# Kernel optimization log

Measured on AMD Instinct MI355X. Metric: run time of the kernel, lower is better.

Reference implementation:

```python
import jax, jax.numpy as jnp
import numpy as np

B, T, IN, H, OUT = 4096, 7, 512, 1024, 512


def setup_inputs() -> dict:
    key = jax.random.key(0)
    ks = jax.random.split(key, 13)
    s = 0.05  # weight init scale to keep gates/tanh unsaturated
    return {
        "x": jax.random.normal(ks[0], (B, T, IN), jnp.float32),
        "W_ih1": jax.random.normal(ks[1], (3 * H, IN), jnp.float32) * s,
        "W_hh1": jax.random.normal(ks[2], (3 * H, H), jnp.float32) * s,
        "b_ih1": jax.random.normal(ks[3], (3 * H,), jnp.float32) * s,
        "b_hh1": jax.random.normal(ks[4], (3 * H,), jnp.float32) * s,
        "W_ih2": jax.random.normal(ks[5], (3 * H, H), jnp.float32) * s,
        "W_hh2": jax.random.normal(ks[6], (3 * H, H), jnp.float32) * s,
        "b_ih2": jax.random.normal(ks[7], (3 * H,), jnp.float32) * s,
        "b_hh2": jax.random.normal(ks[8], (3 * H,), jnp.float32) * s,
        "Wo1": jax.random.normal(ks[9], (OUT, H), jnp.float32) * s,
        "bo1": jax.random.normal(ks[10], (OUT,), jnp.float32) * s,
        "Wo2": jax.random.normal(ks[11], (OUT, H), jnp.float32) * s,
        "bo2": jax.random.normal(ks[12], (OUT,), jnp.float32) * s,
    }


def gru_cell(x, h, W_ih, W_hh, b_ih, b_hh):
    # torch.nn.GRUCell math, gate order (r, z, n)
    gi = x @ W_ih.T + b_ih          # [B, 3H]
    gh = h @ W_hh.T + b_hh          # [B, 3H]
    i_r, i_z, i_n = jnp.split(gi, 3, axis=-1)
    h_r, h_z, h_n = jnp.split(gh, 3, axis=-1)
    r = jax.nn.sigmoid(i_r + h_r)
    z = jax.nn.sigmoid(i_z + h_z)
    n = jnp.tanh(i_n + r * h_n)
    return (1.0 - z) * n + z * h


def reference(x, W_ih1, W_hh1, b_ih1, b_hh1, W_ih2, W_hh2, b_ih2, b_hh2,
              Wo1, bo1, Wo2, bo2):
    batch = x.shape[0]
    h1_0 = jnp.zeros((batch, H), x.dtype)
    h2_0 = jnp.zeros((batch, H), x.dtype)

    def step(carry, x_t):
        h1, h2 = carry
        h1 = gru_cell(x_t, h1, W_ih1, W_hh1, b_ih1, b_hh1)
        h2 = gru_cell(h1, h2, W_ih2, W_hh2, b_ih2, b_hh2)
        out = jnp.tanh(h1 @ Wo1.T + bo1) + jnp.tanh(h2 @ Wo2.T + bo2)
        # s_t_cached starts as T zeros and only T steps run, so the popped
        # cached state is always zeros: mse(h2, 0) == mean(h2**2)
        aux = jnp.mean(jnp.square(h2))
        return (h1, h2), (out, aux)

    xs = jnp.swapaxes(x, 0, 1)  # [T, B, IN]
    _, (outs, auxs) = jax.lax.scan(step, (h1_0, h2_0), xs)
    outputs = jnp.swapaxes(outs, 0, 1)  # [B, T, OUT]
    aux_loss = jnp.sum(auxs)
    return outputs, aux_loss
```

## Files before the change

kernel.cpp:

```cpp
#include <hip/hip_runtime.h>
#include <cstdint>

#define BB   4096
#define TT   7
#define INF  512
#define HH   1024
#define OUTF 512
#define G3   3072

typedef short bf16x8 __attribute__((ext_vector_type(8)));
typedef float f32x4  __attribute__((ext_vector_type(4)));

static __device__ __forceinline__ unsigned short f2bf(float f) {
  unsigned u = __float_as_uint(f);
  unsigned r = ((u >> 16) & 1u) + 0x7FFFu;
  return (unsigned short)((u + r) >> 16);
}
static __device__ __forceinline__ float bf2f(unsigned short s) {
  return __uint_as_float(((unsigned)s) << 16);
}

#define GLDS16(gp, lp)                                                        \
  __builtin_amdgcn_global_load_lds(                                           \
      (const __attribute__((address_space(1))) void*)(gp),                    \
      (__attribute__((address_space(3))) void*)(lp), 16, 0, 0)

__device__ __forceinline__ int xcd_swz(int bid, int nwg) {
  return (bid & 7) * (nwg >> 3) + (bid >> 3);
}

__global__ __launch_bounds__(256)
void cvt_f32_to_bf16_x4(const float* __restrict__ in, unsigned short* __restrict__ out, int n4) {
  int i = blockIdx.x * 256 + threadIdx.x;
  if (i >= n4) return;
  const float4 v = ((const float4*)in)[i];
  ushort4 o;
  o.x = f2bf(v.x); o.y = f2bf(v.y); o.z = f2bf(v.z); o.w = f2bf(v.w);
  ((ushort4*)out)[i] = o;
}

template<int BM, int BN, int WM, int WN, int GN>
__device__ __forceinline__ void gemm_core(
    const unsigned short* __restrict__ A, long lda, long bm,
    const unsigned short* __restrict__ Wp, long ldw, int K,
    const float* __restrict__ biasp,
    void* __restrict__ Cp, long ldc,
    const float* __restrict__ addp, long ldadd, int mode)
{
  constexpr int ABUF = BM * 32;
  constexpr int WBUF = BN * 32;
  constexpr int AR = (BM * 4) / 256;
  constexpr int WR = (BN * 4) / 256;
  __shared__ __attribute__((aligned(16))) unsigned short sm[2 * (ABUF + WBUF)];
  unsigned short* As = sm;
  unsigned short* Ws = sm + 2 * ABUF;
  __attribute__((address_space(3))) unsigned short* lAs =
      (__attribute__((address_space(3))) unsigned short*)As;
  __attribute__((address_space(3))) unsigned short* lWs =
      (__attribute__((address_space(3))) unsigned short*)Ws;

  const int tid  = threadIdx.x;
  const int lane = tid & 63;
  const int wid  = tid >> 6;
  const int wr = (wid / GN) * (WM * 16);
  const int wc = (wid % GN) * (WN * 16);
  const int fr = lane & 15;
  const int fk = (lane >> 4) * 8;

  const unsigned short* gpa[AR];
  const unsigned short* gpw[WR];
  int lofa[AR], lofw[WR];
#pragma unroll
  for (int r = 0; r < AR; ++r) {
    const int c = r * 256 + tid;
    gpa[r] = A + (bm + (c >> 2)) * lda + (c & 3) * 8;
    lofa[r] = c * 8;
  }
#pragma unroll
  for (int r = 0; r < WR; ++r) {
    const int c = r * 256 + tid;
    gpw[r] = Wp + (long)(c >> 2) * ldw + (c & 3) * 8;
    lofw[r] = c * 8;
  }

#define STAGE(buf, kt) do {                                                   \
    _Pragma("unroll")                                                         \
    for (int r = 0; r < AR; ++r) GLDS16(gpa[r] + (kt), lAs + (buf) * ABUF + lofa[r]); \
    _Pragma("unroll")                                                         \
    for (int r = 0; r < WR; ++r) GLDS16(gpw[r] + (kt), lWs + (buf) * WBUF + lofw[r]); \
  } while (0)

  f32x4 acc[WM][WN] = {};
  STAGE(0, 0);
  __syncthreads();
  const int NK = K >> 5;
  for (int it = 0; it < NK; ++it) {
    const int cur = it & 1;
    if (it + 1 < NK) STAGE(cur ^ 1, (it + 1) << 5);
    bf16x8 af[WM], wf[WN];
#pragma unroll
    for (int i = 0; i < WM; ++i)
      af[i] = *(const bf16x8*)&As[cur * ABUF + (wr + i * 16 + fr) * 32 + fk];
#pragma unroll
    for (int i = 0; i < WN; ++i)
      wf[i] = *(const bf16x8*)&Ws[cur * WBUF + (wc + i * 16 + fr) * 32 + fk];
#pragma unroll
    for (int mi = 0; mi < WM; ++mi)
#pragma unroll
      for (int ni = 0; ni < WN; ++ni)
        acc[mi][ni] = __builtin_amdgcn_mfma_f32_16x16x32_bf16(af[mi], wf[ni], acc[mi][ni], 0, 0, 0);
    __syncthreads();
  }
#undef STAGE

  const int q = lane >> 4;
#pragma unroll
  for (int ni = 0; ni < WN; ++ni) {
    const int col = wc + ni * 16 + fr;
    const float bv = biasp[col];
#pragma unroll
    for (int mi = 0; mi < WM; ++mi) {
      const long row = bm + wr + mi * 16 + q * 4;
#pragma unroll
      for (int j = 0; j < 4; ++j) {
        const float v = acc[mi][ni][j] + bv;
        if (mode == 0)      ((float*)Cp)[(row + j) * ldc + col] = v;
        else if (mode == 1) ((float*)Cp)[(row + j) * ldc + col] = tanhf(v);
        else if (mode == 2) ((float*)Cp)[(row + j) * ldc + col] = tanhf(v) + addp[(row + j) * ldadd + col];
        else                ((unsigned short*)Cp)[(row + j) * ldc + col] = f2bf(v);
      }
    }
  }
}

__global__ __launch_bounds__(256)
void k_gi1(const unsigned short* __restrict__ A, long lda,
           const unsigned short* __restrict__ W, const float* __restrict__ bias,
           unsigned short* __restrict__ C, int gx)
{
  const int wg = xcd_swz(blockIdx.x, gridDim.x);
  const int bx = wg % gx, by = wg / gx;
  gemm_core<128,128,4,4,2>(A, lda, (long)bx * 128, W + (long)by * 128 * INF, INF, INF,
                           bias + by * 128, C + by * 128, G3, nullptr, 0, 3);
}

__global__ __launch_bounds__(256)
void k_gh_dual(const unsigned short* __restrict__ h1b, const unsigned short* __restrict__ h2b,
               const unsigned short* __restrict__ W1, const unsigned short* __restrict__ W2,
               const float* __restrict__ b1, const float* __restrict__ b2,
               float* __restrict__ gh1, float* __restrict__ gh2)
{
  const int wg = xcd_swz(blockIdx.x, gridDim.x);
  const int bx = wg % 32;
  const int by = (wg / 32) % 24;
  const int z  = wg / (32 * 24);
  const unsigned short* Aa = z ? h2b : h1b;
  const unsigned short* Ww = (z ? W2 : W1) + (long)by * 128 * HH;
  const float* bias = (z ? b2 : b1) + by * 128;
  float* C = (z ? gh2 : gh1) + by * 128;
  gemm_core<128,128,4,4,2>(Aa, HH, (long)bx * 128, Ww, HH, HH, bias, C, G3, nullptr, 0, 0);
}

__global__ __launch_bounds__(256)
void k_gi2_o1(const unsigned short* __restrict__ h1b,
              const unsigned short* __restrict__ Wih2, const float* __restrict__ bih2,
              float* __restrict__ gi2,
              const unsigned short* __restrict__ Wo1, const float* __restrict__ bo1,
              float* __restrict__ o1t)
{
  const int wg = xcd_swz(blockIdx.x, gridDim.x);
  const int bx = wg % 32;
  const int by = wg / 32;
  const bool g = (by < 24);
  const int bo = by - 24;
  const unsigned short* Ww = g ? (Wih2 + (long)by * 128 * HH) : (Wo1 + (long)bo * 128 * HH);
  const float* bias        = g ? (bih2 + by * 128)            : (bo1 + bo * 128);
  void* C                  = g ? (void*)(gi2 + by * 128)      : (void*)(o1t + bo * 128);
  const long ldc           = g ? (long)G3 : (long)OUTF;
  gemm_core<128,128,4,4,2>(h1b, HH, (long)bx * 128, Ww, HH, HH, bias, C, ldc,
                           nullptr, 0, g ? 0 : 1);
}

__global__ __launch_bounds__(256)
void k_o2_out(const unsigned short* __restrict__ h2b,
              const unsigned short* __restrict__ Wo2, const float* __restrict__ bo2,
              const float* __restrict__ o1t, float* __restrict__ outp)
{
  const int wg = xcd_swz(blockIdx.x, gridDim.x);
  const int bx = wg % 64;
  const int by = wg / 64;
  gemm_core<64,64,2,2,2>(h2b, HH, (long)bx * 64, Wo2 + (long)by * 64 * HH, HH, HH,
                         bo2 + by * 64, outp + by * 64, (long)TT * OUTF,
                         o1t + by * 64, OUTF, 2);
}

template<bool GIBF>
__global__ __launch_bounds__(256)
void k_gate(const void* __restrict__ gi, long gistride,
            const float* __restrict__ gh,
            unsigned short* __restrict__ hb,
            float* __restrict__ auxp)
{
  const int i4 = blockIdx.x * 256 + threadIdx.x;
  const int e  = i4 << 2;
  const int b = e >> 10;
  const int c = e & 1023;
  f32x4 ir, iz, inn;
  if (GIBF) {
    const unsigned short* g = (const unsigned short*)gi + (long)b * gistride + c;
    const ushort4 a0 = *(const ushort4*)(g);
    const ushort4 a1 = *(const ushort4*)(g + HH);
    const ushort4 a2 = *(const ushort4*)(g + 2 * HH);
    ir  = f32x4{bf2f(a0.x), bf2f(a0.y), bf2f(a0.z), bf2f(a0.w)};
    iz  = f32x4{bf2f(a1.x), bf2f(a1.y), bf2f(a1.z), bf2f(a1.w)};
    inn = f32x4{bf2f(a2.x), bf2f(a2.y), bf2f(a2.z), bf2f(a2.w)};
  } else {
    const float* g = (const float*)gi + (long)b * gistride + c;
    ir = *(const f32x4*)g; iz = *(const f32x4*)(g + HH); inn = *(const f32x4*)(g + 2 * HH);
  }
  const float* ghp = gh + (long)b * G3 + c;
  const f32x4 hr = *(const f32x4*)ghp;
  const f32x4 hz = *(const f32x4*)(ghp + HH);
  const f32x4 hn = *(const f32x4*)(ghp + 2 * HH);
  const ushort4 ho = *(const ushort4*)(hb + e);
  const f32x4 h = f32x4{bf2f(ho.x), bf2f(ho.y), bf2f(ho.z), bf2f(ho.w)};
  f32x4 hnew;
  float vsum = 0.f;
#pragma unroll
  for (int j = 0; j < 4; ++j) {
    const float r = 1.f / (1.f + __expf(-(ir[j] + hr[j])));
    const float z = 1.f / (1.f + __expf(-(iz[j] + hz[j])));
    const float n = tanhf(inn[j] + r * hn[j]);
    hnew[j] = (1.f - z) * n + z * h[j];
    vsum += hnew[j] * hnew[j];
  }
  ushort4 o;
  o.x = f2bf(hnew[0]); o.y = f2bf(hnew[1]); o.z = f2bf(hnew[2]); o.w = f2bf(hnew[3]);
  *(ushort4*)(hb + e) = o;
  if (auxp != nullptr) {
#pragma unroll
    for (int off = 32; off > 0; off >>= 1) vsum += __shfl_down(vsum, off);
    __shared__ float wsum[4];
    if ((threadIdx.x & 63) == 0) wsum[threadIdx.x >> 6] = vsum;
    __syncthreads();
    if (threadIdx.x == 0) auxp[blockIdx.x] = wsum[0] + wsum[1] + wsum[2] + wsum[3];
  }
}

__global__ __launch_bounds__(256)
void aux_reduce(const float* __restrict__ p, int n, float* __restrict__ out, float scale) {
  float s = 0.f;
  for (int i = threadIdx.x; i < n; i += 256) s += p[i];
#pragma unroll
  for (int off = 32; off > 0; off >>= 1) s += __shfl_down(s, off);
  __shared__ float wsum[4];
  if ((threadIdx.x & 63) == 0) wsum[threadIdx.x >> 6] = s;
  __syncthreads();
  if (threadIdx.x == 0) out[0] = (wsum[0] + wsum[1] + wsum[2] + wsum[3]) * scale;
}

extern "C" void kernel_launch(void* const* d_in, const int* in_sizes, int n_in,
                              void* d_out, int out_size, void* d_ws, size_t ws_size,
                              hipStream_t stream) {
  const float* x    = (const float*)d_in[0];
  const float* Wih1 = (const float*)d_in[1];
  const float* Whh1 = (const float*)d_in[2];
  const float* bih1 = (const float*)d_in[3];
  const float* bhh1 = (const float*)d_in[4];
  const float* Wih2 = (const float*)d_in[5];
  const float* Whh2 = (const float*)d_in[6];
  const float* bih2 = (const float*)d_in[7];
  const float* bhh2 = (const float*)d_in[8];
  const float* Wo1  = (const float*)d_in[9];
  const float* bo1  = (const float*)d_in[10];
  const float* Wo2  = (const float*)d_in[11];
  const float* bo2  = (const float*)d_in[12];

  char* ws = (char*)d_ws;
  size_t off = 0;
  auto alloc = [&](size_t bytes) {
    char* p = ws + off;
    off = (off + bytes + 255) & ~(size_t)255;
    return p;
  };

  unsigned short* xb    = (unsigned short*)alloc((size_t)BB * TT * INF * 2);
  unsigned short* wih1b = (unsigned short*)alloc((size_t)G3 * INF * 2);
  unsigned short* whh1b = (unsigned short*)alloc((size_t)G3 * HH * 2);
  unsigned short* wih2b = (unsigned short*)alloc((size_t)G3 * HH * 2);
  unsigned short* whh2b = (unsigned short*)alloc((size_t)G3 * HH * 2);
  unsigned short* wo1b  = (unsigned short*)alloc((size_t)OUTF * HH * 2);
  unsigned short* wo2b  = (unsigned short*)alloc((size_t)OUTF * HH * 2);
  unsigned short* h1b = (unsigned short*)alloc((size_t)BB * HH * 2);
  unsigned short* h2b = (unsigned short*)alloc((size_t)BB * HH * 2);
  float* gh1  = (float*)alloc((size_t)BB * G3 * 4);
  float* gh2  = (float*)alloc((size_t)BB * G3 * 4);
  float* o1t  = (float*)alloc((size_t)BB * OUTF * 4);
  float* auxp = (float*)alloc((size_t)TT * (BB * HH / 1024) * 4);
  float* gi2  = gh1;

  const size_t gi1_big   = (size_t)BB * TT * G3 * 2;
  const size_t gi1_small = (size_t)BB * G3 * 2;
  const bool hoist = (off + gi1_big + (size_t)(32 << 20)) <= ws_size;
  unsigned short* gi1b = (unsigned short*)alloc(hoist ? gi1_big : gi1_small);

  float* aux = (float*)d_out + (size_t)BB * TT * OUTF;

  auto cvt = [&](const float* src, unsigned short* dst, size_t n) {
    int n4 = (int)(n / 4);
    cvt_f32_to_bf16_x4<<<dim3((n4 + 255) / 256), dim3(256), 0, stream>>>(src, dst, n4);
  };
  cvt(x,    xb,    (size_t)BB * TT * INF);
  cvt(Wih1, wih1b, (size_t)G3 * INF);
  cvt(Whh1, whh1b, (size_t)G3 * HH);
  cvt(Wih2, wih2b, (size_t)G3 * HH);
  cvt(Whh2, whh2b, (size_t)G3 * HH);
  cvt(Wo1,  wo1b,  (size_t)OUTF * HH);
  cvt(Wo2,  wo2b,  (size_t)OUTF * HH);

  hipMemsetAsync(h1b, 0, (size_t)BB * HH * 2, stream);
  hipMemsetAsync(h2b, 0, (size_t)BB * HH * 2, stream);

  const dim3 blk(256);
  const int gateGrid = BB * HH / 1024;

  if (hoist)
    k_gi1<<<dim3(224 * 24), blk, 0, stream>>>(xb, INF, wih1b, bih1, gi1b, 224);

  for (int t = 0; t < TT; ++t) {
    if (!hoist)
      k_gi1<<<dim3(32 * 24), blk, 0, stream>>>(xb + (size_t)t * INF, (long)TT * INF,
                                               wih1b, bih1, gi1b, 32);
    k_gh_dual<<<dim3(32 * 24 * 2), blk, 0, stream>>>(h1b, h2b, whh1b, whh2b, bhh1, bhh2, gh1, gh2);
    k_gate<true><<<dim3(gateGrid), blk, 0, stream>>>(
        hoist ? gi1b + (size_t)t * G3 : gi1b, hoist ? (long)TT * G3 : (long)G3,
        gh1, h1b, nullptr);
    k_gi2_o1<<<dim3(32 * 28), blk, 0, stream>>>(h1b, wih2b, bih2, gi2, wo1b, bo1, o1t);
    k_gate<false><<<dim3(gateGrid), blk, 0, stream>>>(gi2, (long)G3, gh2, h2b,
                                                      auxp + (size_t)t * gateGrid);
    k_o2_out<<<dim3(64 * 8), blk, 0, stream>>>(h2b, wo2b, bo2, o1t,
                                               (float*)d_out + (size_t)t * OUTF);
  }
  aux_reduce<<<dim3(1), blk, 0, stream>>>(auxp, TT * gateGrid, aux,
                                          1.f / ((float)BB * (float)HH));
}
```

Baseline: 1.568 ms.

## Use single-buffered BK=64 tiles with XOR-swizzled LDS layout in GEMM core

Changes the GEMM mainloop from a double-buffered K=32 pipeline to a single LDS buffer holding K=64 tiles, with two MFMA sub-steps per tile. The global-to-LDS load addresses are XOR-swizzled by row so that the 16-byte fragment reads from LDS avoid bank conflicts on the wider 128-byte rows. This halves the number of barrier iterations and removes bank conflicts, but it gives up overlap of the next tile's load with the current MFMA work, since there is a sync before each load.

```diff
diff --git a/kernel.cpp b/kernel.cpp
--- a/kernel.cpp
+++ b/kernel.cpp
@@ -47,13 +47,11 @@
     void* __restrict__ Cp, long ldc,
     const float* __restrict__ addp, long ldadd, int mode)
 {
-  constexpr int ABUF = BM * 32;
-  constexpr int WBUF = BN * 32;
-  constexpr int AR = (BM * 4) / 256;
-  constexpr int WR = (BN * 4) / 256;
-  __shared__ __attribute__((aligned(16))) unsigned short sm[2 * (ABUF + WBUF)];
+  constexpr int AR = (BM * 8) / 256;
+  constexpr int WR = (BN * 8) / 256;
+  __shared__ __attribute__((aligned(16))) unsigned short sm[(BM + BN) * 64];
   unsigned short* As = sm;
-  unsigned short* Ws = sm + 2 * ABUF;
+  unsigned short* Ws = sm + BM * 64;
   __attribute__((address_space(3))) unsigned short* lAs =
       (__attribute__((address_space(3))) unsigned short*)As;
   __attribute__((address_space(3))) unsigned short* lWs =
@@ -65,53 +63,57 @@
   const int wr = (wid / GN) * (WM * 16);
   const int wc = (wid % GN) * (WN * 16);
   const int fr = lane & 15;
-  const int fk = (lane >> 4) * 8;
+  const int q2 = lane >> 4;
 
   const unsigned short* gpa[AR];
   const unsigned short* gpw[WR];
   int lofa[AR], lofw[WR];
 #pragma unroll
   for (int r = 0; r < AR; ++r) {
-    const int c = r * 256 + tid;
-    gpa[r] = A + (bm + (c >> 2)) * lda + (c & 3) * 8;
-    lofa[r] = c * 8;
+    const int id = r * 256 + tid;
+    const int row = id >> 3, cc = id & 7;
+    gpa[r] = A + (bm + row) * lda + (cc ^ (row & 7)) * 8;
+    lofa[r] = id * 8;
   }
 #pragma unroll
   for (int r = 0; r < WR; ++r) {
-    const int c = r * 256 + tid;
-    gpw[r] = Wp + (long)(c >> 2) * ldw + (c & 3) * 8;
-    lofw[r] = c * 8;
-  }
-
-#define STAGE(buf, kt) do {                                                   \
-    _Pragma("unroll")                                                         \
-    for (int r = 0; r < AR; ++r) GLDS16(gpa[r] + (kt), lAs + (buf) * ABUF + lofa[r]); \
-    _Pragma("unroll")                                                         \
-    for (int r = 0; r < WR; ++r) GLDS16(gpw[r] + (kt), lWs + (buf) * WBUF + lofw[r]); \
-  } while (0)
+    const int id = r * 256 + tid;
+    const int row = id >> 3, cc = id & 7;
+    gpw[r] = Wp + (long)row * ldw + (cc ^ (row & 7)) * 8;
+    lofw[r] = id * 8;
+  }
 
   f32x4 acc[WM][WN] = {};
-  STAGE(0, 0);
-  __syncthreads();
-  const int NK = K >> 5;
-  for (int it = 0; it < NK; ++it) {
-    const int cur = it & 1;
-    if (it + 1 < NK) STAGE(cur ^ 1, (it + 1) << 5);
-    bf16x8 af[WM], wf[WN];
-#pragma unroll
-    for (int i = 0; i < WM; ++i)
-      af[i] = *(const bf16x8*)&As[cur * ABUF + (wr + i * 16 + fr) * 32 + fk];
-#pragma unroll
-    for (int i = 0; i < WN; ++i)
-      wf[i] = *(const bf16x8*)&Ws[cur * WBUF + (wc + i * 16 + fr) * 32 + fk];
-#pragma unroll
-    for (int mi = 0; mi < WM; ++mi)
-#pragma unroll
-      for (int ni = 0; ni < WN; ++ni)
-        acc[mi][ni] = __builtin_amdgcn_mfma_f32_16x16x32_bf16(af[mi], wf[ni], acc[mi][ni], 0, 0, 0);
+  for (int kt = 0; kt < K; kt += 64) {
+    if (kt) __syncthreads();
+#pragma unroll
+    for (int r = 0; r < AR; ++r) GLDS16(gpa[r] + kt, lAs + lofa[r]);
+#pragma unroll
+    for (int r = 0; r < WR; ++r) GLDS16(gpw[r] + kt, lWs + lofw[r]);
     __syncthreads();
-  }
-#undef STAGE
+
+#pragma unroll
+    for (int ks = 0; ks < 2; ++ks) {
+      bf16x8 af[WM], wf[WN];
+#pragma unroll
+      for (int i = 0; i < WM; ++i) {
+        const int row = wr + i * 16 + fr;
+        const int ch  = (ks * 4 + q2) ^ (row & 7);
+        af[i] = *(const bf16x8*)&As[row * 64 + ch * 8];
+      }
+#pragma unroll
+      for (int i = 0; i < WN; ++i) {
+        const int row = wc + i * 16 + fr;
+        const int ch  = (ks * 4 + q2) ^ (row & 7);
+        wf[i] = *(const bf16x8*)&Ws[row * 64 + ch * 8];
+      }
+#pragma unroll
+      for (int mi = 0; mi < WM; ++mi)
+#pragma unroll
+        for (int ni = 0; ni < WN; ++ni)
+          acc[mi][ni] = __builtin_amdgcn_mfma_f32_16x16x32_bf16(af[mi], wf[ni], acc[mi][ni], 0, 0, 0);
+    }
+  }
 
   const int q = lane >> 4;
 #pragma unroll
```

Result: faster. 1.419 ms (-9.5%).
